# Kernel optimization log

Measured on AMD Instinct MI355X. Metric: run time of the kernel, lower is better.

Reference implementation:

```python
import jax, jax.numpy as jnp
import numpy as np

B, S, D, H = 2, 2048, 768, 12
DK = D // H
NEG = -1000000000.0


def setup_inputs() -> dict:
    key = jax.random.key(0)
    ks = jax.random.split(key, 12)
    inp = {
        "query": jax.random.normal(ks[0], (B, S, D), jnp.float32),
        "key": jax.random.normal(ks[1], (B, S, D), jnp.float32),
        "value": jax.random.normal(ks[2], (B, S, D), jnp.float32),
        "mask": jax.random.randint(ks[3], (B, 1, 1, S), 0, 2, jnp.int32),
    }
    sc = 1.0 / np.sqrt(D)
    inp["Wq"] = jax.random.normal(ks[4], (D, D), jnp.float32) * sc
    inp["bq"] = jnp.zeros((D,), jnp.float32)
    inp["Wk"] = jax.random.normal(ks[5], (D, D), jnp.float32) * sc
    inp["bk"] = jnp.zeros((D,), jnp.float32)
    inp["Wv"] = jax.random.normal(ks[6], (D, D), jnp.float32) * sc
    inp["bv"] = jnp.zeros((D,), jnp.float32)
    inp["Wo"] = jax.random.normal(ks[7], (D, D), jnp.float32) * sc
    inp["bo"] = jnp.zeros((D,), jnp.float32)
    return inp


def reference(query, key, value, mask, Wq, bq, Wk, bk, Wv, bv, Wo, bo):
    b = query.shape[0]
    # QKV projections -> [B, H, S, DK]
    def proj(x, W, bias):
        y = jnp.einsum('bsd,de->bse', x, W.T) + bias
        return y.reshape(b, -1, H, DK).transpose(0, 2, 1, 3)
    q = proj(query, Wq, bq)
    k = proj(key, Wk, bk)
    v = proj(value, Wv, bv)
    # scores: [B, H, S, S]
    scores = jnp.einsum('bhqd,bhkd->bhqk', q, k) / jnp.sqrt(jnp.float32(DK))
    scores = jnp.where(mask == 0, jnp.float32(NEG), scores)
    p = jax.nn.softmax(scores, axis=-1)
    x = jnp.einsum('bhqk,bhkd->bhqd', p, v)  # [B, H, S, DK]
    x = x.transpose(0, 2, 1, 3).reshape(b, -1, H * DK)
    return jnp.einsum('bsd,de->bse', x, Wo.T) + bo
```

## Files before the change

### kernel.cpp

```cpp
#include <hip/hip_runtime.h>

typedef unsigned short u16;
typedef __attribute__((ext_vector_type(8))) __bf16 bf16x8;
typedef __attribute__((ext_vector_type(8))) short s16x8;
typedef __attribute__((ext_vector_type(8))) unsigned short u16x8;
typedef __attribute__((ext_vector_type(4))) float f32x4;
typedef __attribute__((ext_vector_type(4))) unsigned short u16x4;
typedef __attribute__((ext_vector_type(4))) float fl4;
typedef __attribute__((ext_vector_type(4))) int i32x4;
typedef __attribute__((ext_vector_type(4))) unsigned char u8x4;

#define MFMA(a, b, c) __builtin_amdgcn_mfma_f32_16x16x32_bf16((a), (b), (c), 0, 0, 0)
#define QSC 0.18033688011112042f

__device__ __forceinline__ u16 f2bf(float f) {
  __bf16 h = (__bf16)f;
  return __builtin_bit_cast(unsigned short, h);
}

__device__ __forceinline__ float bf2f(u16 u) {
  union { unsigned u; float f; } v; v.u = ((unsigned)u) << 16;
  return v.f;
}

__device__ __forceinline__ void gll16(const u16* g, u16* l) {
  typedef __attribute__((address_space(1))) unsigned int gu32;
  typedef __attribute__((address_space(3))) unsigned int lu32;
  __builtin_amdgcn_global_load_lds((gu32*)g, (lu32*)l, 16, 0, 0);
}


__global__ __launch_bounds__(256) void k_convert_w(
    const float* __restrict__ Wq, const float* __restrict__ Wk,
    const float* __restrict__ Wv, const float* __restrict__ Wo,
    u16* __restrict__ wqkv, u16* __restrict__ wob) {
  const int n = 3072 * 192;
  for (int i = blockIdx.x * 256 + threadIdx.x; i < n; i += gridDim.x * 256) {
    int row = i / 192;
    int col = (i - row * 192) * 4;
    const float* src; u16* dst; float sc = 1.0f;
    if (row < 768)       { src = Wq + row * 768;          dst = wqkv + row * 768; sc = QSC; }
    else if (row < 1536) { src = Wk + (row - 768) * 768;  dst = wqkv + row * 768; }
    else if (row < 2304) { src = Wv + (row - 1536) * 768; dst = wqkv + row * 768; }
    else                 { src = Wo + (row - 2304) * 768; dst = wob + (row - 2304) * 768; }
    fl4 f = *(const fl4*)(src + col);
    u16x4 o;
    o[0] = f2bf(f[0] * sc); o[1] = f2bf(f[1] * sc);
    o[2] = f2bf(f[2] * sc); o[3] = f2bf(f[3] * sc);
    *(u16x4*)(dst + col) = o;
  }
}


__global__ __launch_bounds__(256) void k_gemm_qkv(
    const float* __restrict__ xq, const float* __restrict__ xk,
    const float* __restrict__ xv, const u16* __restrict__ wqkv,
    const float* __restrict__ bq, const float* __restrict__ bk_,
    const float* __restrict__ bv_,
    u16* __restrict__ Qb, u16* __restrict__ Kb, u16* __restrict__ Vtb) {
  __shared__ __align__(16) u16 Abuf[2][64 * 32];
  __shared__ __align__(16) u16 Bbuf[2][128 * 32];
  const int tid = threadIdx.x;
  const int bid = blockIdx.x;
  const int wid = (bid & 7) * 144 + (bid >> 3);
  const int row0 = (wid / 18) * 64, col0 = (wid % 18) * 128;
  const int seg = col0 / 768;
  const float* A32 = (seg == 0) ? xq : ((seg == 1) ? xk : xv);
  const int w = tid >> 6, lane = tid & 63, lr = lane & 15, kg = lane >> 4;
  const int wr = (w >> 1) * 32, wc = (w & 1) * 64;

  const int c0 = tid, c1 = tid + 256;
  const int r0c = c0 >> 2, g0 = (c0 & 3) ^ ((r0c >> 1) & 3);
  const int r1c = c1 >> 2, g1 = (c1 & 3) ^ ((r1c >> 1) & 3);
  const float* aS0 = A32 + (size_t)(row0 + r0c) * 768 + g0 * 8;
  const u16* bS0 = wqkv + (size_t)(col0 + r0c) * 768 + g0 * 8;
  const u16* bS1 = wqkv + (size_t)(col0 + r1c) * 768 + g1 * 8;

  f32x4 acc[2][4];
  f32x4 zero = {0.f, 0.f, 0.f, 0.f};
#pragma unroll
  for (int i = 0; i < 2; i++)
#pragma unroll
    for (int j = 0; j < 4; j++) acc[i][j] = zero;

  int aoff[2], boff[4];
#pragma unroll
  for (int mi = 0; mi < 2; mi++) {
    int r = wr + mi * 16 + lr;
    aoff[mi] = r * 32 + (kg ^ ((r >> 1) & 3)) * 8;
  }
#pragma unroll
  for (int ni = 0; ni < 4; ni++) {
    int r = wc + ni * 16 + lr;
    boff[ni] = r * 32 + (kg ^ ((r >> 1) & 3)) * 8;
  }

  fl4 ar[2];
#define LOADA(kt) { ar[0] = *(const fl4*)(aS0 + (kt) * 32);       \
                    ar[1] = *(const fl4*)(aS0 + (kt) * 32 + 4); }
#define WRITEA(buf) { u16x8 t0;                                   \
    t0[0]=f2bf(ar[0][0]); t0[1]=f2bf(ar[0][1]); t0[2]=f2bf(ar[0][2]); t0[3]=f2bf(ar[0][3]); \
    t0[4]=f2bf(ar[1][0]); t0[5]=f2bf(ar[1][1]); t0[6]=f2bf(ar[1][2]); t0[7]=f2bf(ar[1][3]); \
    *(u16x8*)((buf) + c0 * 8) = t0; }
#define STAGEB(kt, buf) { gll16(bS0 + (kt) * 32, (buf) + c0 * 8); \
                          gll16(bS1 + (kt) * 32, (buf) + c1 * 8); }

  LOADA(0);
  STAGEB(0, Bbuf[0]);
  WRITEA(Abuf[0]);
  __syncthreads();

  for (int kt = 0; kt < 24; kt++) {
    const int cur = kt & 1;
    if (kt < 23) { LOADA(kt + 1); STAGEB(kt + 1, Bbuf[cur ^ 1]); }
    bf16x8 af[2], bfr[4];
#pragma unroll
    for (int mi = 0; mi < 2; mi++) af[mi] = *(const bf16x8*)(Abuf[cur] + aoff[mi]);
#pragma unroll
    for (int ni = 0; ni < 4; ni++) bfr[ni] = *(const bf16x8*)(Bbuf[cur] + boff[ni]);
#pragma unroll
    for (int mi = 0; mi < 2; mi++)
#pragma unroll
      for (int ni = 0; ni < 4; ni++)
        acc[mi][ni] = MFMA(af[mi], bfr[ni], acc[mi][ni]);
    __syncthreads();
    if (kt < 23) {
      WRITEA(Abuf[cur ^ 1]);
      __syncthreads();
    }
  }
#undef LOADA
#undef WRITEA
#undef STAGEB

  const float* bias = (seg == 0) ? bq : ((seg == 1) ? bk_ : bv_);
  const float bsc = (seg == 0) ? QSC : 1.0f;
  const int ncol0 = col0 - seg * 768;
#pragma unroll
  for (int ni = 0; ni < 4; ni++) {
    const int n = ncol0 + wc + ni * 16 + lr;
    const float bval = bias[n] * bsc;
    const int hh = n >> 6, dk = n & 63;
#pragma unroll
    for (int mi = 0; mi < 2; mi++)
#pragma unroll
      for (int j = 0; j < 4; j++) {
        const int m = row0 + wr + mi * 16 + kg * 4 + j;
        const int bb = m >> 11, ss = m & 2047;
        const u16 val = f2bf(acc[mi][ni][j] + bval);
        if (seg == 0)
          Qb[((size_t)((bb * 12 + hh) * 2048 + ss)) * 64 + dk] = val;
        else if (seg == 1)
          Kb[((size_t)((bb * 12 + hh) * 2048 + ss)) * 64 + dk] = val;
        else
          Vtb[((size_t)((bb * 12 + hh) * 64 + dk)) * 2048 + ss] = val;
      }
  }
}


__global__ __launch_bounds__(256) void k_attn(
    const u16* __restrict__ Qb, const u16* __restrict__ Kb,
    const u16* __restrict__ Vtb, const int* __restrict__ mask,
    u16* __restrict__ o_part, float* __restrict__ l_part) {
  __shared__ __align__(16) u16 Ks[2][64 * 64];
  __shared__ __align__(16) u16 Vs[2][64 * 64];
  __shared__ __align__(16) u16 Ps[4][32 * 64];
  __shared__ __align__(4) unsigned char mlds8[1024];
  const int bid = blockIdx.x;
  const int wid = (bid & 7) * 96 + (bid >> 3);
  const int qt = wid & 15;
  const int gh = wid >> 4;
  const int bh = gh >> 1, half = gh & 1;
  const int b = bh / 12;
  const int kvb = half << 10;
  const int tid = threadIdx.x, w = tid >> 6, lane = tid & 63;
  const int lr = lane & 15, g = lane >> 4;
  const int q0 = qt * 128 + w * 32;
  const u16* Qh = Qb + (size_t)bh * (2048 * 64);
  const u16* Kh = Kb + (size_t)bh * (2048 * 64);
  const u16* Vh = Vtb + (size_t)bh * (64 * 2048);
  const int* mb = mask + b * 2048;
  u16* Pw = Ps[w];

  {
    i32x4 m4 = *(const i32x4*)(mb + kvb + tid * 4);
    u8x4 m8;
    m8[0] = (unsigned char)m4[0]; m8[1] = (unsigned char)m4[1];
    m8[2] = (unsigned char)m4[2]; m8[3] = (unsigned char)m4[3];
    *(u8x4*)(mlds8 + tid * 4) = m8;
  }

  bf16x8 aq[2][2];
#pragma unroll
  for (int mi = 0; mi < 2; mi++)
#pragma unroll
    for (int ks = 0; ks < 2; ks++)
      aq[mi][ks] = *(const bf16x8*)(Qh + (q0 + mi * 16 + lr) * 64 + ks * 32 + g * 8);

  f32x4 zero = {0.f, 0.f, 0.f, 0.f};
  f32x4 o[2][4];
#pragma unroll
  for (int mi = 0; mi < 2; mi++)
#pragma unroll
    for (int di = 0; di < 4; di++) o[mi][di] = zero;
  f32x4 o_l[2];
  o_l[0] = zero; o_l[1] = zero;

  s16x8 ov = {0x3F80, 0x3F80, 0x3F80, 0x3F80, 0x3F80, 0x3F80, 0x3F80, 0x3F80};
  bf16x8 ones = __builtin_bit_cast(bf16x8, ov);

  const int c0 = tid, c1 = tid + 256;
  const int sr0 = c0 >> 3, sg0 = (c0 & 7) ^ (sr0 & 7);
  const int sr1 = c1 >> 3, sg1 = (c1 & 7) ^ (sr1 & 7);
  const u16* kA0 = Kh + (size_t)kvb * 64 + sr0 * 64 + sg0 * 8;
  const u16* kA1 = Kh + (size_t)kvb * 64 + sr1 * 64 + sg1 * 8;
  const u16* vA0 = Vh + sr0 * 2048 + kvb + sg0 * 8;
  const u16* vA1 = Vh + sr1 * 2048 + kvb + sg1 * 8;

#define STAGE(u) { u16* kd = Ks[(u)&1]; u16* vd = Vs[(u)&1];           \
    gll16(kA0 + (u) * 4096, kd + c0 * 8);                              \
    gll16(kA1 + (u) * 4096, kd + c1 * 8);                              \
    gll16(vA0 + (u) * 64,  vd + c0 * 8);                               \
    gll16(vA1 + (u) * 64,  vd + c1 * 8); }

  STAGE(0);
  __syncthreads();

  for (int t = 0; t < 16; t++) {
    if (t < 15) STAGE(t + 1);
    const u16* Kc = Ks[t & 1];
    const u16* Vc = Vs[t & 1];

    f32x4 s[2][4];
#pragma unroll
    for (int ni = 0; ni < 4; ni++) {
      const int row = ni * 16 + lr;
      bf16x8 b0 = *(const bf16x8*)(Kc + row * 64 + ((g ^ (row & 7)) << 3));
      bf16x8 b1 = *(const bf16x8*)(Kc + row * 64 + (((4 + g) ^ (row & 7)) << 3));
#pragma unroll
      for (int mi = 0; mi < 2; mi++) {
        f32x4 z = MFMA(b0, aq[mi][0], zero);
        z = MFMA(b1, aq[mi][1], z);
        s[mi][ni] = z;
      }
    }
#pragma unroll
    for (int ni = 0; ni < 4; ni++) {
      const u8x4 mk4 = *(const u8x4*)(mlds8 + t * 64 + ni * 16 + g * 4);
#pragma unroll
      for (int mi = 0; mi < 2; mi++)
#pragma unroll
        for (int j = 0; j < 4; j++)
          s[mi][ni][j] = mk4[j] ? s[mi][ni][j] : -1e9f;
    }

#pragma unroll
    for (int mi = 0; mi < 2; mi++) {
      const int prow = mi * 16 + lr;
      const int rbase = prow * 128, sw = (prow & 7) << 4;
#pragma unroll
      for (int ni = 0; ni < 4; ni++) {
        u16x4 pk;
#pragma unroll
        for (int j = 0; j < 4; j++)
          pk[j] = f2bf(__builtin_amdgcn_exp2f(s[mi][ni][j]));
        *(u16x4*)(Pw + ((rbase + ((ni * 32 + g * 8) ^ sw)) >> 1)) = pk;
      }
    }

#pragma unroll
    for (int ks2 = 0; ks2 < 2; ks2++) {
      bf16x8 ap[2];
#pragma unroll
      for (int mi = 0; mi < 2; mi++) {
        const int prow = mi * 16 + lr;
        const int byt = prow * 128 + ((ks2 * 64 + g * 16) ^ ((prow & 7) << 4));
        ap[mi] = *(const bf16x8*)(Pw + (byt >> 1));
      }
#pragma unroll
      for (int di = 0; di < 4; di++) {
        const int vrow = di * 16 + lr;
        bf16x8 bv = *(const bf16x8*)(Vc + vrow * 64 + (((ks2 * 4 + g) ^ (vrow & 7)) << 3));
#pragma unroll
        for (int mi = 0; mi < 2; mi++)
          o[mi][di] = MFMA(ap[mi], bv, o[mi][di]);
      }
#pragma unroll
      for (int mi = 0; mi < 2; mi++)
        o_l[mi] = MFMA(ap[mi], ones, o_l[mi]);
    }

    if (t < 15) __syncthreads();
  }
#undef STAGE

  u16* opw = o_part + (size_t)(half * 24 + bh) * (2048 * 64);
  float* lpw = l_part + (size_t)(half * 24 + bh) * 2048;
#pragma unroll
  for (int mi = 0; mi < 2; mi++) {
#pragma unroll
    for (int di = 0; di < 4; di++)
#pragma unroll
      for (int j = 0; j < 4; j++) {
        const int row = q0 + mi * 16 + g * 4 + j;
        opw[(size_t)row * 64 + di * 16 + lr] = f2bf(o[mi][di][j]);
      }
    if (lr == 0) {
#pragma unroll
      for (int j = 0; j < 4; j++)
        lpw[q0 + mi * 16 + g * 4 + j] = o_l[mi][j];
    }
  }
}


__global__ __launch_bounds__(256) void k_combine(
    const u16* __restrict__ o_part, const float* __restrict__ l_part,
    u16* __restrict__ attn) {
  const int idx = blockIdx.x * 256 + threadIdx.x;
  const int row = idx >> 3;
  const int c8 = (idx & 7) << 3;
  const size_t HALF_O = (size_t)24 * 2048 * 64;
  u16x8 a0 = *(const u16x8*)(o_part + (size_t)row * 64 + c8);
  u16x8 a1 = *(const u16x8*)(o_part + HALF_O + (size_t)row * 64 + c8);
  const float l = l_part[row] + l_part[24 * 2048 + row];
  const float rcp = 1.0f / l;
  u16x8 r;
#pragma unroll
  for (int j = 0; j < 8; j++)
    r[j] = f2bf((bf2f(a0[j]) + bf2f(a1[j])) * rcp);
  const int bh = row >> 11, s = row & 2047;
  const int b = bh / 12, h = bh - b * 12;
  *(u16x8*)(attn + (size_t)(b * 2048 + s) * 768 + h * 64 + c8) = r;
}


__global__ __launch_bounds__(256) void k_gemm_out(
    const u16* __restrict__ attn, const u16* __restrict__ wob,
    const float* __restrict__ bo, float* __restrict__ out) {
  __shared__ __align__(16) u16 As[2][128 * 32];
  __shared__ __align__(16) u16 Bs[2][128 * 32];
  const int tid = threadIdx.x;
  const int bid = blockIdx.x;
  const int wid = (bid & 7) * 24 + (bid >> 3);
  const int row0 = (wid / 6) * 128, col0 = (wid % 6) * 128;
  const int w = tid >> 6, lane = tid & 63, lr = lane & 15, kg = lane >> 4;
  const int wr = (w >> 1) * 64, wc = (w & 1) * 64;

  const int c0 = tid, c1 = tid + 256;
  const int r0c = c0 >> 2, g0 = (c0 & 3) ^ ((r0c >> 1) & 3);
  const int r1c = c1 >> 2, g1 = (c1 & 3) ^ ((r1c >> 1) & 3);
  const u16* aS0 = attn + (size_t)(row0 + r0c) * 768 + g0 * 8;
  const u16* aS1 = attn + (size_t)(row0 + r1c) * 768 + g1 * 8;
  const u16* bS0 = wob + (size_t)(col0 + r0c) * 768 + g0 * 8;
  const u16* bS1 = wob + (size_t)(col0 + r1c) * 768 + g1 * 8;

  f32x4 acc[4][4];
  f32x4 zero = {0.f, 0.f, 0.f, 0.f};
#pragma unroll
  for (int i = 0; i < 4; i++)
#pragma unroll
    for (int j = 0; j < 4; j++) acc[i][j] = zero;

  int aoff[4], boff[4];
#pragma unroll
  for (int mi = 0; mi < 4; mi++) {
    int r = wr + mi * 16 + lr;
    aoff[mi] = r * 32 + (kg ^ ((r >> 1) & 3)) * 8;
  }
#pragma unroll
  for (int ni = 0; ni < 4; ni++) {
    int r = wc + ni * 16 + lr;
    boff[ni] = r * 32 + (kg ^ ((r >> 1) & 3)) * 8;
  }

#define STAGE(kt) { u16* ad = As[(kt)&1]; u16* bd = Bs[(kt)&1];   \
    gll16(aS0 + (kt) * 32, ad + c0 * 8);                          \
    gll16(aS1 + (kt) * 32, ad + c1 * 8);                          \
    gll16(bS0 + (kt) * 32, bd + c0 * 8);                          \
    gll16(bS1 + (kt) * 32, bd + c1 * 8); }

  STAGE(0);
  __syncthreads();

  for (int kt = 0; kt < 24; kt++) {
    const int cur = kt & 1;
    if (kt < 23) STAGE(kt + 1);
    bf16x8 af[4], bfr[4];
#pragma unroll
    for (int mi = 0; mi < 4; mi++) af[mi] = *(const bf16x8*)(As[cur] + aoff[mi]);
#pragma unroll
    for (int ni = 0; ni < 4; ni++) bfr[ni] = *(const bf16x8*)(Bs[cur] + boff[ni]);
#pragma unroll
    for (int mi = 0; mi < 4; mi++)
#pragma unroll
      for (int ni = 0; ni < 4; ni++)
        acc[mi][ni] = MFMA(af[mi], bfr[ni], acc[mi][ni]);
    if (kt < 23) __syncthreads();
  }
#undef STAGE

#pragma unroll
  for (int ni = 0; ni < 4; ni++) {
    const int n = col0 + wc + ni * 16 + lr;
    const float bval = bo[n];
#pragma unroll
    for (int mi = 0; mi < 4; mi++)
#pragma unroll
      for (int j = 0; j < 4; j++) {
        const int m = row0 + wr + mi * 16 + kg * 4 + j;
        out[(size_t)m * 768 + n] = acc[mi][ni][j] + bval;
      }
  }
}


extern "C" void kernel_launch(void* const* d_in, const int* in_sizes, int n_in,
                              void* d_out, int out_size, void* d_ws, size_t ws_size,
                              hipStream_t stream) {
  const float* q = (const float*)d_in[0];
  const float* k = (const float*)d_in[1];
  const float* v = (const float*)d_in[2];
  const int* mask = (const int*)d_in[3];
  const float* Wq = (const float*)d_in[4];
  const float* bq = (const float*)d_in[5];
  const float* Wk = (const float*)d_in[6];
  const float* bk = (const float*)d_in[7];
  const float* Wv = (const float*)d_in[8];
  const float* bv = (const float*)d_in[9];
  const float* Wo = (const float*)d_in[10];
  const float* bo = (const float*)d_in[11];
  float* out = (float*)d_out;

  u16* scratch = (u16*)d_ws;
  u16* wqkv = scratch + (size_t)3 * 4096 * 768;
  u16* wob = wqkv + (size_t)2304 * 768;
  u16* Qb = wob + (size_t)768 * 768;
  u16* Kb = Qb + (size_t)4096 * 768;
  u16* Vtb = Kb + (size_t)4096 * 768;
  u16* attn = Vtb + (size_t)4096 * 768;

  u16* o_part = scratch;
  float* l_part = (float*)(scratch + (size_t)2 * 24 * 2048 * 64);

  k_convert_w<<<dim3(2304), dim3(256), 0, stream>>>(Wq, Wk, Wv, Wo, wqkv, wob);
  k_gemm_qkv<<<dim3(1152), dim3(256), 0, stream>>>(q, k, v, wqkv, bq, bk, bv, Qb, Kb, Vtb);
  k_attn<<<dim3(768), dim3(256), 0, stream>>>(Qb, Kb, Vtb, mask, o_part, l_part);
  k_combine<<<dim3(1536), dim3(256), 0, stream>>>(o_part, l_part, attn);
  k_gemm_out<<<dim3(192), dim3(256), 0, stream>>>(attn, wob, bo, out);
}
```

Before: 110.4 us.

## Stage fp32 activations via direct global-to-LDS loads and convert when reading fragments

The QKV projection GEMM now stages the fp32 A tile straight into LDS with the same async global-to-LDS loads used for B, using a new XOR swizzle for the 16-byte float chunks. Conversion to bf16 moves to fragment-read time. This drops the register round trip and the second barrier per k-step. The cost is twice the LDS footprint for A and twice the LDS read traffic, plus conversion work repeated by each wave that reads the same rows.

```diff
diff --git a/kernel.cpp b/kernel.cpp
--- a/kernel.cpp
+++ b/kernel.cpp
@@ -58,7 +58,7 @@
     const float* __restrict__ bq, const float* __restrict__ bk_,
     const float* __restrict__ bv_,
     u16* __restrict__ Qb, u16* __restrict__ Kb, u16* __restrict__ Vtb) {
-  __shared__ __align__(16) u16 Abuf[2][64 * 32];
+  __shared__ __align__(16) float Af[2][64 * 32];
   __shared__ __align__(16) u16 Bbuf[2][128 * 32];
   const int tid = threadIdx.x;
   const int bid = blockIdx.x;
@@ -70,11 +70,14 @@
   const int wr = (w >> 1) * 32, wc = (w & 1) * 64;
 
   const int c0 = tid, c1 = tid + 256;
-  const int r0c = c0 >> 2, g0 = (c0 & 3) ^ ((r0c >> 1) & 3);
-  const int r1c = c1 >> 2, g1 = (c1 & 3) ^ ((r1c >> 1) & 3);
-  const float* aS0 = A32 + (size_t)(row0 + r0c) * 768 + g0 * 8;
-  const u16* bS0 = wqkv + (size_t)(col0 + r0c) * 768 + g0 * 8;
-  const u16* bS1 = wqkv + (size_t)(col0 + r1c) * 768 + g1 * 8;
+  const int arow0 = c0 >> 3, ag0 = (c0 & 7) ^ (arow0 & 7);
+  const int arow1 = c1 >> 3, ag1 = (c1 & 7) ^ (arow1 & 7);
+  const float* aS0 = A32 + (size_t)(row0 + arow0) * 768 + ag0 * 4;
+  const float* aS1 = A32 + (size_t)(row0 + arow1) * 768 + ag1 * 4;
+  const int br0 = c0 >> 2, bg0 = (c0 & 3) ^ ((br0 >> 1) & 3);
+  const int br1 = c1 >> 2, bg1 = (c1 & 3) ^ ((br1 >> 1) & 3);
+  const u16* bS0 = wqkv + (size_t)(col0 + br0) * 768 + bg0 * 8;
+  const u16* bS1 = wqkv + (size_t)(col0 + br1) * 768 + bg1 * 8;
 
   f32x4 acc[2][4];
   f32x4 zero = {0.f, 0.f, 0.f, 0.f};
@@ -83,11 +86,12 @@
 #pragma unroll
     for (int j = 0; j < 4; j++) acc[i][j] = zero;
 
-  int aoff[2], boff[4];
+  int aoffL[2], aoffH[2], boff[4];
 #pragma unroll
   for (int mi = 0; mi < 2; mi++) {
     int r = wr + mi * 16 + lr;
-    aoff[mi] = r * 32 + (kg ^ ((r >> 1) & 3)) * 8;
+    aoffL[mi] = r * 32 + ((2 * kg) ^ (r & 7)) * 4;
+    aoffH[mi] = r * 32 + ((2 * kg + 1) ^ (r & 7)) * 4;
   }
 #pragma unroll
   for (int ni = 0; ni < 4; ni++) {
@@ -95,27 +99,28 @@
     boff[ni] = r * 32 + (kg ^ ((r >> 1) & 3)) * 8;
   }
 
-  fl4 ar[2];
-#define LOADA(kt) { ar[0] = *(const fl4*)(aS0 + (kt) * 32);       \
-                    ar[1] = *(const fl4*)(aS0 + (kt) * 32 + 4); }
-#define WRITEA(buf) { u16x8 t0;                                   \
-    t0[0]=f2bf(ar[0][0]); t0[1]=f2bf(ar[0][1]); t0[2]=f2bf(ar[0][2]); t0[3]=f2bf(ar[0][3]); \
-    t0[4]=f2bf(ar[1][0]); t0[5]=f2bf(ar[1][1]); t0[6]=f2bf(ar[1][2]); t0[7]=f2bf(ar[1][3]); \
-    *(u16x8*)((buf) + c0 * 8) = t0; }
-#define STAGEB(kt, buf) { gll16(bS0 + (kt) * 32, (buf) + c0 * 8); \
-                          gll16(bS1 + (kt) * 32, (buf) + c1 * 8); }
-
-  LOADA(0);
-  STAGEB(0, Bbuf[0]);
-  WRITEA(Abuf[0]);
+#define STAGE(kt) { u16* ad = (u16*)Af[(kt)&1]; u16* bd = Bbuf[(kt)&1];   \
+    gll16((const u16*)(aS0 + (kt) * 32), ad + c0 * 8);                    \
+    gll16((const u16*)(aS1 + (kt) * 32), ad + c1 * 8);                    \
+    gll16(bS0 + (kt) * 32, bd + c0 * 8);                                  \
+    gll16(bS1 + (kt) * 32, bd + c1 * 8); }
+
+  STAGE(0);
   __syncthreads();
 
   for (int kt = 0; kt < 24; kt++) {
     const int cur = kt & 1;
-    if (kt < 23) { LOADA(kt + 1); STAGEB(kt + 1, Bbuf[cur ^ 1]); }
+    if (kt < 23) STAGE(kt + 1);
     bf16x8 af[2], bfr[4];
 #pragma unroll
-    for (int mi = 0; mi < 2; mi++) af[mi] = *(const bf16x8*)(Abuf[cur] + aoff[mi]);
+    for (int mi = 0; mi < 2; mi++) {
+      fl4 lo = *(const fl4*)(Af[cur] + aoffL[mi]);
+      fl4 hi = *(const fl4*)(Af[cur] + aoffH[mi]);
+      u16x8 t;
+      t[0] = f2bf(lo[0]); t[1] = f2bf(lo[1]); t[2] = f2bf(lo[2]); t[3] = f2bf(lo[3]);
+      t[4] = f2bf(hi[0]); t[5] = f2bf(hi[1]); t[6] = f2bf(hi[2]); t[7] = f2bf(hi[3]);
+      af[mi] = __builtin_bit_cast(bf16x8, t);
+    }
 #pragma unroll
     for (int ni = 0; ni < 4; ni++) bfr[ni] = *(const bf16x8*)(Bbuf[cur] + boff[ni]);
 #pragma unroll
@@ -123,15 +128,9 @@
 #pragma unroll
       for (int ni = 0; ni < 4; ni++)
         acc[mi][ni] = MFMA(af[mi], bfr[ni], acc[mi][ni]);
-    __syncthreads();
-    if (kt < 23) {
-      WRITEA(Abuf[cur ^ 1]);
-      __syncthreads();
-    }
-  }
-#undef LOADA
-#undef WRITEA
-#undef STAGEB
+    if (kt < 23) __syncthreads();
+  }
+#undef STAGE
 
   const float* bias = (seg == 0) ? bq : ((seg == 1) ? bk_ : bv_);
   const float bsc = (seg == 0) ? QSC : 1.0f;
```

Result: slower. 119.8 us (+8.4%).
